# Kernel optimization log

Measured on AMD Instinct MI355X. Metric: run time of the kernel, lower is better.

## Reference

```python
import jax, jax.numpy as jnp
import numpy as np


def setup_inputs() -> dict:
    key = jax.random.key(0)
    k1, k2, k3, k4 = jax.random.split(key, 4)
    B, C_in, KH, KW, C_out = 256, 512, 7, 7, 1000
    inputR = jax.random.normal(k1, (B, C_in, KH, KW), dtype=jnp.float32)
    inputSPD = jax.random.normal(k2, (B, C_in, C_in), dtype=jnp.float32)
    fan_in = C_in * KH * KW
    weight = jax.random.normal(k3, (C_out, C_in, KH, KW), dtype=jnp.float32) / np.sqrt(fan_in)
    bias = jax.random.normal(k4, (C_out,), dtype=jnp.float32) / np.sqrt(fan_in)
    return {"inputR": inputR, "inputSPD": inputSPD, "weight": weight, "bias": bias}


def reference(inputR, inputSPD, weight, bias):
    # Conv2d with kernel == spatial size and padding 0 == fully connected layer.
    # outputR: (N, C_out)
    outputR = jnp.einsum('nchw,ochw->no', inputR, weight) + bias

    # top-2 channel selection per sample (indices only; values unused)
    _, top2_idx = jax.lax.top_k(outputR, 2)  # (N, 2)

    # weight is detached for the SPD path in the original module
    w_spd = jax.lax.stop_gradient(weight)[top2_idx]  # (N, 2, C_in, KH, KW)

    # outputSPD[n,k,m] = sum_{c,d,h,w} SPD[n,c,d] * W2[n,k,d,h,w] * W2[n,m,c,h,w]
    # (equivalent to the original's two batched matmuls + sum over (h, w))
    outputSPD = jnp.einsum('ncd,nkdhw,nmchw->nkm', inputSPD, w_spd, w_spd)  # (N, 2, 2)
    return outputR, outputSPD
```

## Files before the change

### kernel.cpp

```cpp
#include <hip/hip_runtime.h>

#define KD 25088
#define N_DIM 1000
#define ZS 28

typedef __attribute__((ext_vector_type(8))) short bf16x8;
typedef __attribute__((ext_vector_type(4))) float f32x4;

__device__ inline unsigned pack2(float a, float b) {
  unsigned r;
  asm("v_cvt_pk_bf16_f32 %0, %1, %2" : "=v"(r) : "v"(a), "v"(b));
  return r;
}
__device__ inline unsigned short f2bf(float x) {
  unsigned r;
  asm("v_cvt_pk_bf16_f32 %0, %1, %1" : "=v"(r) : "v"(x));
  return (unsigned short)r;
}
__device__ inline float bf2f(unsigned short u) {
  union { unsigned u; float f; } v; v.u = ((unsigned)u) << 16; return v.f;
}

__global__ __launch_bounds__(256) void init_bias_k(
    const float* __restrict__ bias, float* __restrict__ outR) {
  const int id = blockIdx.x * 256 + threadIdx.x;
  if (id < 256 * N_DIM) outR[id] = bias[id % N_DIM];
}

__global__ __launch_bounds__(256) void reduce_k(
    const float* __restrict__ part, const float* __restrict__ bias,
    float* __restrict__ outR) {
  const int t4 = blockIdx.x * 256 + threadIdx.x;
  const int e0 = t4 * 4;
  const int n0 = e0 % N_DIM;
  float4 acc = *(const float4*)(bias + n0);
#pragma unroll
  for (int z = 0; z < ZS; ++z) {
    const float4 pv = *(const float4*)(part + (size_t)z * 256 * N_DIM + e0);
    acc.x += pv.x; acc.y += pv.y; acc.z += pv.z; acc.w += pv.w;
  }
  *(float4*)(outR + e0) = acc;
}

template<int ATOMIC>
__global__ __launch_bounds__(256) void rgemm_k(
    const float* __restrict__ A, const float* __restrict__ W,
    float* __restrict__ D) {
  __shared__ unsigned short As[2][128 * 32];
  __shared__ unsigned short Bs[2][128 * 32];
  const int t = threadIdx.x;
  const int id  = blockIdx.x;
  const int mz  = (id & 7) * 7 + ((id >> 3) >> 3);
  const int n0  = ((id >> 3) & 7) * 128;
  const int m0  = (mz / ZS) * 128;
  const int z   = mz % ZS;
  const int lane = t & 63, w = t >> 6;
  const int cw = (w >> 1) * 64, jw = (w & 1) * 64;
  const int r16 = lane & 15, quad = lane >> 4;
  const int srow = t >> 2;
  const int sc8  = (t & 3) << 3;
  const bool doj3 = (n0 + jw + 48) < N_DIM;

  float a_pre[16], b_pre[16];

  f32x4 acc[4][4];
#pragma unroll
  for (int i = 0; i < 4; ++i)
#pragma unroll
    for (int j = 0; j < 4; ++j) {
      acc[i][j][0] = 0.f; acc[i][j][1] = 0.f;
      acc[i][j][2] = 0.f; acc[i][j][3] = 0.f;
    }

#define RG_LOAD(s_)                                                         \
  {                                                                         \
    const int kbase = ((z) * ZS + (s_)) * 32;                               \
    _Pragma("unroll")                                                       \
    for (int h = 0; h < 2; ++h) {                                           \
      const int row = h * 64 + srow;                                        \
      const float* pa = A + (size_t)(m0 + row) * KD + kbase + sc8;          \
      *(float4*)&a_pre[h * 8 + 0] = *(const float4*)pa;                     \
      *(float4*)&a_pre[h * 8 + 4] = *(const float4*)(pa + 4);               \
      const int wr = n0 + row;                                              \
      if (wr < N_DIM) {                                                     \
        const float* pw = W + (size_t)wr * KD + kbase + sc8;                \
        *(float4*)&b_pre[h * 8 + 0] = *(const float4*)pw;                   \
        *(float4*)&b_pre[h * 8 + 4] = *(const float4*)(pw + 4);             \
      } else {                                                              \
        _Pragma("unroll")                                                   \
        for (int q = 0; q < 8; ++q) b_pre[h * 8 + q] = 0.f;                 \
      }                                                                     \
    }                                                                       \
  }

#define RG_WRITE(p_)                                                        \
  {                                                                         \
    _Pragma("unroll")                                                       \
    for (int h = 0; h < 2; ++h) {                                           \
      const int row = h * 64 + srow;                                        \
      uint4 ua, ub;                                                         \
      ua.x = pack2(a_pre[h*8+0], a_pre[h*8+1]);                             \
      ua.y = pack2(a_pre[h*8+2], a_pre[h*8+3]);                             \
      ua.z = pack2(a_pre[h*8+4], a_pre[h*8+5]);                             \
      ua.w = pack2(a_pre[h*8+6], a_pre[h*8+7]);                             \
      ub.x = pack2(b_pre[h*8+0], b_pre[h*8+1]);                             \
      ub.y = pack2(b_pre[h*8+2], b_pre[h*8+3]);                             \
      ub.z = pack2(b_pre[h*8+4], b_pre[h*8+5]);                             \
      ub.w = pack2(b_pre[h*8+6], b_pre[h*8+7]);                             \
      *(uint4*)&As[p_][row * 32 + sc8] = ua;                                \
      *(uint4*)&Bs[p_][row * 32 + sc8] = ub;                                \
    }                                                                       \
  }

  RG_LOAD(0); RG_WRITE(0); __syncthreads();
  int p = 0;
  for (int s = 0; s < ZS; ++s) {
    if (s + 1 < ZS) RG_LOAD(s + 1);
    bf16x8 af[4], bq[4];
#pragma unroll
    for (int i = 0; i < 4; ++i) {
      af[i] = *(const bf16x8*)&As[p][(cw + i * 16 + r16) * 32 + quad * 8];
      if (i < 3 || doj3)
        bq[i] = *(const bf16x8*)&Bs[p][(jw + i * 16 + r16) * 32 + quad * 8];
    }
#pragma unroll
    for (int i = 0; i < 4; ++i)
#pragma unroll
      for (int j = 0; j < 4; ++j)
        if (j < 3 || doj3)
          acc[i][j] = __builtin_amdgcn_mfma_f32_16x16x32_bf16(af[i], bq[j], acc[i][j], 0, 0, 0);
    if (s + 1 < ZS) RG_WRITE(p ^ 1);
    __syncthreads();
    p ^= 1;
  }

#pragma unroll
  for (int j = 0; j < 4; ++j) {
    const int n = n0 + jw + j * 16 + r16;
    if (n < N_DIM) {
#pragma unroll
      for (int i = 0; i < 4; ++i)
#pragma unroll
        for (int r = 0; r < 4; ++r) {
          const int m = m0 + cw + i * 16 + quad * 4 + r;
          if (ATOMIC)
            atomicAdd(&D[(size_t)m * N_DIM + n], acc[i][j][r]);
          else
            D[((size_t)z * 256 + m) * N_DIM + n] = acc[i][j][r];
        }
    }
  }
#undef RG_LOAD
#undef RG_WRITE
}

__global__ __launch_bounds__(64) void top8_k(
    const float* __restrict__ outR, int* __restrict__ top2,
    int* __restrict__ candIdx, int* __restrict__ flags,
    float* __restrict__ outSPD) {
  const int n = blockIdx.x;
  const int lane = threadIdx.x;
  float v[16];
#pragma unroll
  for (int r = 0; r < 16; ++r) {
    const int o = lane + r * 64;
    v[r] = (o < N_DIM) ? outR[(size_t)n * N_DIM + o] : -3.0e38f;
  }
  float cv[8]; int ci[8];
#pragma unroll
  for (int rr = 0; rr < 8; ++rr) {
    float bv = -3.0e38f; int bi = 0x3fffffff;
#pragma unroll
    for (int r = 0; r < 16; ++r) {
      const int o = lane + r * 64;
      if (v[r] > bv || (v[r] == bv && o < bi)) { bv = v[r]; bi = o; }
    }
#pragma unroll
    for (int off = 32; off >= 1; off >>= 1) {
      const float ov = __shfl_xor(bv, off, 64);
      const int   oi = __shfl_xor(bi, off, 64);
      if (ov > bv || (ov == bv && oi < bi)) { bv = ov; bi = oi; }
    }
    cv[rr] = bv; ci[rr] = bi;
#pragma unroll
    for (int r = 0; r < 16; ++r)
      if (lane + r * 64 == bi) v[r] = -3.0e38f;
  }
  if (lane == 0) {
    const bool safe = (cv[0] - cv[1] >= 0.025f) &&
                      (cv[1] - cv[2] >= 0.025f) &&
                      (cv[1] - cv[7] >= 0.05f);
    flags[n] = safe ? 0 : 1;
    top2[2 * n]     = ci[0];
    top2[2 * n + 1] = ci[1];
#pragma unroll
    for (int r = 0; r < 8; ++r) candIdx[n * 8 + r] = ci[r];
    outSPD[4 * n + 0] = 0.f; outSPD[4 * n + 1] = 0.f;
    outSPD[4 * n + 2] = 0.f; outSPD[4 * n + 3] = 0.f;
  }
}

__global__ __launch_bounds__(256) void rdot_k(
    const float* __restrict__ A, const float* __restrict__ W,
    const float* __restrict__ bias, const int* __restrict__ candIdx,
    const int* __restrict__ flags, float* __restrict__ vals) {
  const int n = blockIdx.x;
  if (!flags[n]) return;
  const int c = blockIdx.y;
  const int idx = candIdx[n * 8 + c];
  const float4* a4 = (const float4*)(A + (size_t)n * KD);
  const float4* w4 = (const float4*)(W + (size_t)idx * KD);
  float s = 0.f;
  for (int i = threadIdx.x; i < KD / 4; i += 256) {
    const float4 av = a4[i];
    const float4 wv = w4[i];
    s += av.x * wv.x + av.y * wv.y + av.z * wv.z + av.w * wv.w;
  }
#pragma unroll
  for (int off = 32; off >= 1; off >>= 1) s += __shfl_xor(s, off, 64);
  __shared__ float red[4];
  const int lane = threadIdx.x & 63, w = threadIdx.x >> 6;
  if (lane == 0) red[w] = s;
  __syncthreads();
  if (threadIdx.x == 0)
    vals[n * 8 + c] = red[0] + red[1] + red[2] + red[3] + bias[idx];
}

__global__ __launch_bounds__(64) void select_k(
    const float* __restrict__ vals, const int* __restrict__ candIdx,
    const int* __restrict__ flags, int* __restrict__ top2) {
  const int n = blockIdx.x;
  if (threadIdx.x != 0 || !flags[n]) return;
  int b0 = -1; float v0 = -3.0e38f; int i0 = 0x3fffffff;
  for (int c = 0; c < 8; ++c) {
    const int idx = candIdx[n * 8 + c];
    const float vv = vals[n * 8 + c];
    if (vv > v0 || (vv == v0 && idx < i0)) { v0 = vv; i0 = idx; b0 = c; }
  }
  float v1 = -3.0e38f; int i1 = 0x3fffffff;
  for (int c = 0; c < 8; ++c) {
    if (c == b0) continue;
    const int idx = candIdx[n * 8 + c];
    const float vv = vals[n * 8 + c];
    if (vv > v1 || (vv == v1 && idx < i1)) { v1 = vv; i1 = idx; }
  }
  top2[2 * n]     = i0;
  top2[2 * n + 1] = i1;
}

__global__ __launch_bounds__(256) void packsel_k(
    const float* __restrict__ W, const int* __restrict__ candIdx,
    const int* __restrict__ flags, const float* __restrict__ vals,
    unsigned short* __restrict__ Wp) {
  __shared__ unsigned short tile[49 * 130];
  __shared__ int sel_s;
  const int n = blockIdx.x;
  const int which = blockIdx.y;
  const int t = threadIdx.x;
  if (t == 0) {
    int ia, ib;
    if (!flags[n]) {
      ia = candIdx[n * 8];
      ib = candIdx[n * 8 + 1];
    } else {
      int b0 = -1; float v0 = -3.0e38f; int i0 = 0x3fffffff;
      for (int c = 0; c < 8; ++c) {
        const int idx = candIdx[n * 8 + c];
        const float vv = vals[n * 8 + c];
        if (vv > v0 || (vv == v0 && idx < i0)) { v0 = vv; i0 = idx; b0 = c; }
      }
      float v1 = -3.0e38f; int i1 = 0x3fffffff;
      for (int c = 0; c < 8; ++c) {
        if (c == b0) continue;
        const int idx = candIdx[n * 8 + c];
        const float vv = vals[n * 8 + c];
        if (vv > v1 || (vv == v1 && idx < i1)) { v1 = vv; i1 = idx; }
      }
      ia = i0; ib = i1;
    }
    sel_s = which ? ib : ia;
  }
  unsigned short* dstn = Wp + (size_t)n * 65536;
  {
    const int r0 = 98 + which * 15;
    for (int u = t; u < 15 * 128; u += 256) {
      const int rr = u >> 7;
      const int cc = (u & 127) << 1;
      *(unsigned*)(dstn + (size_t)(r0 + rr) * 512 + cc) = 0u;
    }
  }
  __syncthreads();
  const int sel = sel_s;
  const float4* src4 = (const float4*)(W + (size_t)sel * KD);
  for (int chunk = 0; chunk < 4; ++chunk) {
    const float4* s4 = src4 + chunk * 1568;
    for (int u4 = t; u4 < 1568; u4 += 256) {
      const float4 fv = s4[u4];
      const float vv[4] = {fv.x, fv.y, fv.z, fv.w};
      const int i0 = u4 * 4;
#pragma unroll
      for (int e = 0; e < 4; ++e) {
        const int idx = i0 + e;
        const int c = idx / 49;
        const int hw = idx - c * 49;
        tile[hw * 130 + c] = f2bf(vv[e]);
      }
    }
    __syncthreads();
    const int cp = t & 63, hwb = t >> 6;
    unsigned short* wbase = dstn + (size_t)which * 49 * 512 + chunk * 128 + 2 * cp;
#pragma unroll
    for (int it = 0; it < 13; ++it) {
      const int hw = hwb + it * 4;
      if (hw < 49) {
        const unsigned val = *(const unsigned*)&tile[hw * 130 + 2 * cp];
        *(unsigned*)(wbase + (size_t)hw * 512) = val;
      }
    }
    __syncthreads();
  }
}

__global__ __launch_bounds__(256) void spd_k(
    const float* __restrict__ S, const unsigned short* __restrict__ Wp,
    float* __restrict__ outSPD) {
  __shared__ unsigned short As[2][128 * 32];
  __shared__ float red[4];
  const int t = threadIdx.x;
  const int id = blockIdx.x;
  const int n  = (id & 7) * 32 + ((id >> 3) >> 2);
  const int c0 = ((id >> 3) & 3) * 128;
  const float* Sn = S + (size_t)n * 512 * 512;
  const unsigned short* Wpn = Wp + (size_t)n * 65536;
  const int lane = t & 63, w = t >> 6;
  const int cw = (w >> 1) * 64, jw = (w & 1) * 64;
  const int r16 = lane & 15, quad = lane >> 4;
  const int srow = t >> 2;
  const int sc8  = (t & 3) << 3;
  const bool doj3 = (jw == 0);

  if (t < 4) red[t] = 0.f;

  float a_pre[16];

  f32x4 acc[4][4];
#pragma unroll
  for (int i = 0; i < 4; ++i)
#pragma unroll
    for (int j = 0; j < 4; ++j) {
      acc[i][j][0] = 0.f; acc[i][j][1] = 0.f;
      acc[i][j][2] = 0.f; acc[i][j][3] = 0.f;
    }

  const unsigned short* wjb[4];
#pragma unroll
  for (int j = 0; j < 4; ++j)
    wjb[j] = Wpn + (size_t)(jw + j * 16 + r16) * 512 + quad * 8;

#define SP_LOAD(s_)                                                         \
  {                                                                         \
    const int d0 = (s_) * 32;                                               \
    _Pragma("unroll")                                                       \
    for (int h = 0; h < 2; ++h) {                                           \
      const int row = h * 64 + srow;                                        \
      const float* pa = Sn + (size_t)(c0 + row) * 512 + d0 + sc8;           \
      *(float4*)&a_pre[h * 8 + 0] = *(const float4*)pa;                     \
      *(float4*)&a_pre[h * 8 + 4] = *(const float4*)(pa + 4);               \
    }                                                                       \
  }

#define SP_WRITE(p_)                                                        \
  {                                                                         \
    _Pragma("unroll")                                                       \
    for (int h = 0; h < 2; ++h) {                                           \
      const int row = h * 64 + srow;                                        \
      uint4 ua;                                                             \
      ua.x = pack2(a_pre[h*8+0], a_pre[h*8+1]);                             \
      ua.y = pack2(a_pre[h*8+2], a_pre[h*8+3]);                             \
      ua.z = pack2(a_pre[h*8+4], a_pre[h*8+5]);                             \
      ua.w = pack2(a_pre[h*8+6], a_pre[h*8+7]);                             \
      *(uint4*)&As[p_][row * 32 + sc8] = ua;                                \
    }                                                                       \
  }

  SP_LOAD(0); SP_WRITE(0); __syncthreads();
  int p = 0;
  for (int s = 0; s < 16; ++s) {
    if (s + 1 < 16) SP_LOAD(s + 1);
    const int k0 = s * 32;
    bf16x8 af[4], bq[4];
#pragma unroll
    for (int i = 0; i < 4; ++i) {
      af[i] = *(const bf16x8*)&As[p][(cw + i * 16 + r16) * 32 + quad * 8];
      if (i < 3 || doj3)
        bq[i] = *(const bf16x8*)(wjb[i] + k0);
    }
#pragma unroll
    for (int i = 0; i < 4; ++i)
#pragma unroll
      for (int j = 0; j < 4; ++j)
        if (j < 3 || doj3)
          acc[i][j] = __builtin_amdgcn_mfma_f32_16x16x32_bf16(af[i], bq[j], acc[i][j], 0, 0, 0);
    if (s + 1 < 16) SP_WRITE(p ^ 1);
    __syncthreads();
    p ^= 1;
  }
#undef SP_LOAD
#undef SP_WRITE

  float p00 = 0.f, p01 = 0.f, p10 = 0.f, p11 = 0.f;
#pragma unroll
  for (int j = 0; j < 4; ++j) {
    const int jj = jw + j * 16 + r16;
    if (jj < 98) {
      const int kk = (jj >= 49);
      const int hw = jj - 49 * kk;
      const unsigned short* wa = Wpn + (size_t)hw * 512;
      const unsigned short* wb = Wpn + (size_t)(49 + hw) * 512;
#pragma unroll
      for (int i = 0; i < 4; ++i) {
#pragma unroll
        for (int r = 0; r < 4; ++r) {
          const int c = c0 + cw + i * 16 + quad * 4 + r;
          const float u   = acc[i][j][r];
          const float wav = bf2f(wa[c]);
          const float wbv = bf2f(wb[c]);
          if (kk == 0) { p00 = fmaf(u, wav, p00); p01 = fmaf(u, wbv, p01); }
          else         { p10 = fmaf(u, wav, p10); p11 = fmaf(u, wbv, p11); }
        }
      }
    }
  }

  atomicAdd(&red[0], p00);
  atomicAdd(&red[1], p01);
  atomicAdd(&red[2], p10);
  atomicAdd(&red[3], p11);
  __syncthreads();
  if (t < 4) atomicAdd(&outSPD[n * 4 + t], red[t]);
}

__global__ __launch_bounds__(256) void spd_fb_k(
    const float* __restrict__ S, const float* __restrict__ W,
    const int* __restrict__ top2, float* __restrict__ outSPD) {
  __shared__ unsigned short As[128 * 40];
  __shared__ unsigned short Bs[128 * 40];
  __shared__ float red[4];
  const int t = threadIdx.x;
  const int n  = blockIdx.x >> 2;
  const int c0 = (blockIdx.x & 3) * 128;
  const int ia = top2[2 * n];
  const int ib = top2[2 * n + 1];
  const float* Sn = S + (size_t)n * 512 * 512;
  const int lane = t & 63, w = t >> 6;
  const int cw = (w >> 1) * 64, jw = (w & 1) * 64;
  const int r16 = lane & 15, quad = lane >> 4;
  if (t < 4) red[t] = 0.f;
  f32x4 acc[4][4];
#pragma unroll
  for (int i = 0; i < 4; ++i)
#pragma unroll
    for (int j = 0; j < 4; ++j) {
      acc[i][j][0] = 0.f; acc[i][j][1] = 0.f;
      acc[i][j][2] = 0.f; acc[i][j][3] = 0.f;
    }
  const int bj  = t & 127;
  const int bh  = t >> 7;
  const int bkk = (bj >= 49);
  const int bhw = bj - 49 * bkk;
  const bool bvalid = (bj < 98);
  const float* brow = W + (size_t)(bkk ? ib : ia) * KD + bhw;
  for (int d0 = 0; d0 < 512; d0 += 32) {
#pragma unroll
    for (int h = 0; h < 4; ++h) {
      const int idx = h * 256 + t;
      const int row = idx >> 3;
      const int c4  = (idx & 7) << 2;
      float4 av = *(const float4*)(Sn + (size_t)(c0 + row) * 512 + d0 + c4);
      uint2 pa;
      pa.x = pack2(av.x, av.y);
      pa.y = pack2(av.z, av.w);
      *(uint2*)&As[row * 40 + c4] = pa;
    }
#pragma unroll
    for (int dd2 = 0; dd2 < 16; dd2 += 2) {
      const int dd = bh * 16 + dd2;
      const float x0 = bvalid ? brow[(size_t)(d0 + dd) * 49] : 0.f;
      const float x1 = bvalid ? brow[(size_t)(d0 + dd + 1) * 49] : 0.f;
      *(unsigned*)&Bs[bj * 40 + dd] = pack2(x0, x1);
    }
    __syncthreads();
    bf16x8 af[4], bq[4];
#pragma unroll
    for (int i = 0; i < 4; ++i) {
      af[i] = *(const bf16x8*)&As[(cw + i * 16 + r16) * 40 + quad * 8];
      bq[i] = *(const bf16x8*)&Bs[(jw + i * 16 + r16) * 40 + quad * 8];
    }
#pragma unroll
    for (int i = 0; i < 4; ++i)
#pragma unroll
      for (int j = 0; j < 4; ++j)
        acc[i][j] = __builtin_amdgcn_mfma_f32_16x16x32_bf16(af[i], bq[j], acc[i][j], 0, 0, 0);
    __syncthreads();
  }
  float p00 = 0.f, p01 = 0.f, p10 = 0.f, p11 = 0.f;
  const float* Wa = W + (size_t)ia * KD;
  const float* Wb = W + (size_t)ib * KD;
#pragma unroll
  for (int j = 0; j < 4; ++j) {
    const int jj = jw + j * 16 + r16;
    if (jj < 98) {
      const int kk = (jj >= 49);
      const int hw = jj - 49 * kk;
#pragma unroll
      for (int i = 0; i < 4; ++i)
#pragma unroll
        for (int r = 0; r < 4; ++r) {
          const int c = c0 + cw + i * 16 + quad * 4 + r;
          const float u  = acc[i][j][r];
          const float wa = Wa[(size_t)c * 49 + hw];
          const float wb = Wb[(size_t)c * 49 + hw];
          if (kk == 0) { p00 = fmaf(u, wa, p00); p01 = fmaf(u, wb, p01); }
          else         { p10 = fmaf(u, wa, p10); p11 = fmaf(u, wb, p11); }
        }
    }
  }
  atomicAdd(&red[0], p00);
  atomicAdd(&red[1], p01);
  atomicAdd(&red[2], p10);
  atomicAdd(&red[3], p11);
  __syncthreads();
  if (t < 4) atomicAdd(&outSPD[n * 4 + t], red[t]);
}

extern "C" void kernel_launch(void* const* d_in, const int* in_sizes, int n_in,
                              void* d_out, int out_size, void* d_ws, size_t ws_size,
                              hipStream_t stream) {
  const float* inputR   = (const float*)d_in[0];
  const float* inputSPD = (const float*)d_in[1];
  const float* weight   = (const float*)d_in[2];
  const float* bias     = (const float*)d_in[3];
  float* out = (float*)d_out;

  int*   top2    = (int*)d_ws;
  int*   candIdx = (int*)((char*)d_ws + 2048);
  int*   flags   = (int*)((char*)d_ws + 2048 + 8192);
  float* vals    = (float*)((char*)d_ws + 2048 + 8192 + 1024);
  float* part    = (float*)((char*)d_ws + 65536);
  const size_t PART_BYTES = (size_t)ZS * 256 * N_DIM * 4;
  unsigned short* Wp = (unsigned short*)((char*)d_ws + 65536 + PART_BYTES);
  const bool bigws = ws_size >= 65536ull + PART_BYTES + 256ull * 65536ull * 2ull;

  if (bigws) {
    rgemm_k<0><<<dim3(448), 256, 0, stream>>>(inputR, weight, part);
    reduce_k<<<dim3(250), 256, 0, stream>>>(part, bias, out);
    top8_k<<<dim3(256), 64, 0, stream>>>(out, top2, candIdx, flags, out + 256000);
    rdot_k<<<dim3(256, 8), 256, 0, stream>>>(inputR, weight, bias, candIdx, flags, vals);
    packsel_k<<<dim3(256, 2), 256, 0, stream>>>(weight, candIdx, flags, vals, Wp);
    spd_k<<<dim3(1024), 256, 0, stream>>>(inputSPD, Wp, out + 256000);
  } else {
    init_bias_k<<<dim3(1000), 256, 0, stream>>>(bias, out);
    rgemm_k<1><<<dim3(448), 256, 0, stream>>>(inputR, weight, out);
    top8_k<<<dim3(256), 64, 0, stream>>>(out, top2, candIdx, flags, out + 256000);
    rdot_k<<<dim3(256, 8), 256, 0, stream>>>(inputR, weight, bias, candIdx, flags, vals);
    select_k<<<dim3(256), 64, 0, stream>>>(vals, candIdx, flags, top2);
    spd_fb_k<<<dim3(1024), 256, 0, stream>>>(inputSPD, weight, top2, out + 256000);
  }
}
```

Measured before the change: 532.2 us.

## Fuse split-K reduction, top-8 selection and fp32 rescoring into one kernel

Replaces the separate reduce, top-8, rescoring-dot and in-packer reselection kernels with a single per-sample kernel. It sums the split-K partials plus bias into shared memory, writes outR, picks the top-8 candidates, and when the margins are small recomputes fp32 dots to choose the top-2. The packer then just reads top2. The rgemm block-to-tile mapping is also reordered so the two M tiles alternate fastest. This removes three launches and the global round-trips of outR, candidates, flags and vals, but the rescoring dots now run with only 4 waves per sample.

After: 571.8 us. 7.4% more time.

```diff
diff --git a/kernel.cpp b/kernel.cpp
--- a/kernel.cpp
+++ b/kernel.cpp
@@ -25,21 +25,6 @@
     const float* __restrict__ bias, float* __restrict__ outR) {
   const int id = blockIdx.x * 256 + threadIdx.x;
   if (id < 256 * N_DIM) outR[id] = bias[id % N_DIM];
-}
-
-__global__ __launch_bounds__(256) void reduce_k(
-    const float* __restrict__ part, const float* __restrict__ bias,
-    float* __restrict__ outR) {
-  const int t4 = blockIdx.x * 256 + threadIdx.x;
-  const int e0 = t4 * 4;
-  const int n0 = e0 % N_DIM;
-  float4 acc = *(const float4*)(bias + n0);
-#pragma unroll
-  for (int z = 0; z < ZS; ++z) {
-    const float4 pv = *(const float4*)(part + (size_t)z * 256 * N_DIM + e0);
-    acc.x += pv.x; acc.y += pv.y; acc.z += pv.z; acc.w += pv.w;
-  }
-  *(float4*)(outR + e0) = acc;
 }
 
 template<int ATOMIC>
@@ -50,10 +35,11 @@
   __shared__ unsigned short Bs[2][128 * 32];
   const int t = threadIdx.x;
   const int id  = blockIdx.x;
-  const int mz  = (id & 7) * 7 + ((id >> 3) >> 3);
-  const int n0  = ((id >> 3) & 7) * 128;
-  const int m0  = (mz / ZS) * 128;
-  const int z   = mz % ZS;
+  const int loc = id >> 3;
+  const int mzp = (id & 7) * 7 + (loc >> 3);
+  const int n0  = (loc & 7) * 128;
+  const int m0  = (mzp & 1) * 128;
+  const int z   = mzp >> 1;
   const int lane = t & 63, w = t >> 6;
   const int cw = (w >> 1) * 64, jw = (w & 1) * 64;
   const int r16 = lane & 15, quad = lane >> 4;
@@ -154,6 +140,113 @@
 #undef RG_WRITE
 }
 
+__global__ __launch_bounds__(256) void rtop_k(
+    const float* __restrict__ part, const float* __restrict__ A,
+    const float* __restrict__ W, const float* __restrict__ bias,
+    float* __restrict__ outR, int* __restrict__ top2,
+    float* __restrict__ outSPD) {
+  __shared__ float row[1024];
+  __shared__ float cvs[8];
+  __shared__ int   cis[8];
+  __shared__ float dots[8];
+  __shared__ int   flag_s;
+  const int n = blockIdx.x;
+  const int t = threadIdx.x;
+
+  if (t < 250) {
+    const int e0 = t * 4;
+    float4 acc = *(const float4*)(bias + e0);
+#pragma unroll
+    for (int z = 0; z < ZS; ++z) {
+      const float4 pv = *(const float4*)(part + ((size_t)z * 256 + n) * N_DIM + e0);
+      acc.x += pv.x; acc.y += pv.y; acc.z += pv.z; acc.w += pv.w;
+    }
+    *(float4*)(row + e0) = acc;
+    *(float4*)(outR + (size_t)n * N_DIM + e0) = acc;
+  }
+  __syncthreads();
+
+  if (t < 64) {
+    const int lane = t;
+    float v[16];
+#pragma unroll
+    for (int r = 0; r < 16; ++r) {
+      const int o = lane + r * 64;
+      v[r] = (o < N_DIM) ? row[o] : -3.0e38f;
+    }
+    float cv[8]; int ci[8];
+#pragma unroll
+    for (int rr = 0; rr < 8; ++rr) {
+      float bv = -3.0e38f; int bi = 0x3fffffff;
+#pragma unroll
+      for (int r = 0; r < 16; ++r) {
+        const int o = lane + r * 64;
+        if (v[r] > bv || (v[r] == bv && o < bi)) { bv = v[r]; bi = o; }
+      }
+#pragma unroll
+      for (int off = 32; off >= 1; off >>= 1) {
+        const float ov = __shfl_xor(bv, off, 64);
+        const int   oi = __shfl_xor(bi, off, 64);
+        if (ov > bv || (ov == bv && oi < bi)) { bv = ov; bi = oi; }
+      }
+      cv[rr] = bv; ci[rr] = bi;
+#pragma unroll
+      for (int r = 0; r < 16; ++r)
+        if (lane + r * 64 == bi) v[r] = -3.0e38f;
+    }
+    if (lane == 0) {
+      const bool safe = (cv[0] - cv[1] >= 0.025f) &&
+                        (cv[1] - cv[2] >= 0.025f) &&
+                        (cv[1] - cv[7] >= 0.05f);
+      flag_s = safe ? 0 : 1;
+      top2[2 * n]     = ci[0];
+      top2[2 * n + 1] = ci[1];
+#pragma unroll
+      for (int r = 0; r < 8; ++r) { cis[r] = ci[r]; cvs[r] = cv[r]; }
+      outSPD[4 * n + 0] = 0.f; outSPD[4 * n + 1] = 0.f;
+      outSPD[4 * n + 2] = 0.f; outSPD[4 * n + 3] = 0.f;
+    }
+  }
+  __syncthreads();
+
+  if (flag_s) {
+    const int lane = t & 63, w = t >> 6;
+    const float4* a4 = (const float4*)(A + (size_t)n * KD);
+    for (int cc = w; cc < 8; cc += 4) {
+      const int idx = cis[cc];
+      const float4* w4 = (const float4*)(W + (size_t)idx * KD);
+      float s = 0.f;
+      for (int i = lane; i < KD / 4; i += 64) {
+        const float4 av = a4[i];
+        const float4 wv = w4[i];
+        s += av.x * wv.x + av.y * wv.y + av.z * wv.z + av.w * wv.w;
+      }
+#pragma unroll
+      for (int off = 32; off >= 1; off >>= 1) s += __shfl_xor(s, off, 64);
+      if (lane == 0) dots[cc] = s + bias[idx];
+    }
+  }
+  __syncthreads();
+
+  if (flag_s && t == 0) {
+    int b0 = -1; float v0 = -3.0e38f; int i0 = 0x3fffffff;
+    for (int c = 0; c < 8; ++c) {
+      const int idx = cis[c];
+      const float vv = dots[c];
+      if (vv > v0 || (vv == v0 && idx < i0)) { v0 = vv; i0 = idx; b0 = c; }
+    }
+    float v1 = -3.0e38f; int i1 = 0x3fffffff;
+    for (int c = 0; c < 8; ++c) {
+      if (c == b0) continue;
+      const int idx = cis[c];
+      const float vv = dots[c];
+      if (vv > v1 || (vv == v1 && idx < i1)) { v1 = vv; i1 = idx; }
+    }
+    top2[2 * n]     = i0;
+    top2[2 * n + 1] = i1;
+  }
+}
+
 __global__ __launch_bounds__(64) void top8_k(
     const float* __restrict__ outR, int* __restrict__ top2,
     int* __restrict__ candIdx, int* __restrict__ flags,
@@ -249,37 +342,13 @@
 }
 
 __global__ __launch_bounds__(256) void packsel_k(
-    const float* __restrict__ W, const int* __restrict__ candIdx,
-    const int* __restrict__ flags, const float* __restrict__ vals,
+    const float* __restrict__ W, const int* __restrict__ top2,
     unsigned short* __restrict__ Wp) {
   __shared__ unsigned short tile[49 * 130];
-  __shared__ int sel_s;
   const int n = blockIdx.x;
   const int which = blockIdx.y;
   const int t = threadIdx.x;
-  if (t == 0) {
-    int ia, ib;
-    if (!flags[n]) {
-      ia = candIdx[n * 8];
-      ib = candIdx[n * 8 + 1];
-    } else {
-      int b0 = -1; float v0 = -3.0e38f; int i0 = 0x3fffffff;
-      for (int c = 0; c < 8; ++c) {
-        const int idx = candIdx[n * 8 + c];
-        const float vv = vals[n * 8 + c];
-        if (vv > v0 || (vv == v0 && idx < i0)) { v0 = vv; i0 = idx; b0 = c; }
-      }
-      float v1 = -3.0e38f; int i1 = 0x3fffffff;
-      for (int c = 0; c < 8; ++c) {
-        if (c == b0) continue;
-        const int idx = candIdx[n * 8 + c];
-        const float vv = vals[n * 8 + c];
-        if (vv > v1 || (vv == v1 && idx < i1)) { v1 = vv; i1 = idx; }
-      }
-      ia = i0; ib = i1;
-    }
-    sel_s = which ? ib : ia;
-  }
+  const int sel = top2[2 * n + which];
   unsigned short* dstn = Wp + (size_t)n * 65536;
   {
     const int r0 = 98 + which * 15;
@@ -289,8 +358,6 @@
       *(unsigned*)(dstn + (size_t)(r0 + rr) * 512 + cc) = 0u;
     }
   }
-  __syncthreads();
-  const int sel = sel_s;
   const float4* src4 = (const float4*)(W + (size_t)sel * KD);
   for (int chunk = 0; chunk < 4; ++chunk) {
     const float4* s4 = src4 + chunk * 1568;
@@ -553,10 +620,8 @@
 
   if (bigws) {
     rgemm_k<0><<<dim3(448), 256, 0, stream>>>(inputR, weight, part);
-    reduce_k<<<dim3(250), 256, 0, stream>>>(part, bias, out);
-    top8_k<<<dim3(256), 64, 0, stream>>>(out, top2, candIdx, flags, out + 256000);
-    rdot_k<<<dim3(256, 8), 256, 0, stream>>>(inputR, weight, bias, candIdx, flags, vals);
-    packsel_k<<<dim3(256, 2), 256, 0, stream>>>(weight, candIdx, flags, vals, Wp);
+    rtop_k<<<dim3(256), 256, 0, stream>>>(part, inputR, weight, bias, out, top2, out + 256000);
+    packsel_k<<<dim3(256, 2), 256, 0, stream>>>(weight, top2, Wp);
     spd_k<<<dim3(1024), 256, 0, stream>>>(inputSPD, Wp, out + 256000);
   } else {
     init_bias_k<<<dim3(1000), 256, 0, stream>>>(bias, out);
```
